# Performance work log

Measured on AMD Instinct MI355X. Metric: run time of the kernel, lower is better.

The kernel has to match this reference:

```python
import jax, jax.numpy as jnp
import numpy as np

N, T, DM = 8192, 32, 128   # nodes, patches, d_model (d_in = T*DM = 4096)
M, NNZ = 1024, 131072      # hyperedges, incidences
EPS = 1e-5
SLOPE = 0.2


def _bn(x, g, b, axes):
    # BatchNorm with batch statistics (training-mode math, eval dropout)
    m = jnp.mean(x, axis=axes, keepdims=True)
    v = jnp.var(x, axis=axes, keepdims=True)
    return (x - m) / jnp.sqrt(v + EPS) * g + b


def _hconv(x, he_attr, he_n, he_e, W, att, bias, heads):
    # PyG HypergraphConv, use_attention=True, attention_mode='node', concat=False
    out = W.shape[1] // heads
    xt = (x @ W).reshape(N, heads, out)          # [N, H, F]
    et = (he_attr @ W).reshape(M, heads, out)    # [M, H, F]
    xi = xt[he_n]                                # [nnz, H, F] gather node feats
    ej = et[he_e]                                # [nnz, H, F] gather edge feats
    alpha = jnp.sum(jnp.concatenate([xi, ej], axis=-1) * att, axis=-1)  # [nnz, H]
    alpha = jax.nn.leaky_relu(alpha, SLOPE)
    # segment softmax grouped by hyperedge (attention_mode='node')
    amax = jax.ops.segment_max(alpha, he_e, num_segments=M)
    ex = jnp.exp(alpha - amax[he_e])
    alpha = ex / jax.ops.segment_sum(ex, he_e, num_segments=M)[he_e]
    # degree normalizers (hyperedge_weight == 1)
    ones = jnp.ones((NNZ,), x.dtype)
    Dn = jax.ops.segment_sum(ones, he_n, num_segments=N)
    Dinv = jnp.where(Dn > 0, 1.0 / Dn, 0.0)
    Bm = jax.ops.segment_sum(ones, he_e, num_segments=M)
    Binv = jnp.where(Bm > 0, 1.0 / Bm, 0.0)
    # node -> edge, then edge -> node message passing
    eo = jax.ops.segment_sum(alpha[:, :, None] * Binv[he_e][:, None, None] * xi,
                             he_e, num_segments=M)                     # [M, H, F]
    no = jax.ops.segment_sum(alpha[:, :, None] * Dinv[he_n][:, None, None] * eo[he_e],
                             he_n, num_segments=N)                     # [N, H, F]
    return no.mean(axis=1) + bias  # concat=False -> mean over heads


def setup_inputs() -> dict:
    key = jax.random.key(0)
    ks = jax.random.split(key, 16)
    d_in = T * DM
    s = 0.02
    inp = {
        "x": jax.random.normal(ks[0], (N, T, DM), jnp.float32),
        "he_nodes": jax.random.randint(ks[1], (NNZ,), 0, N),
        "he_edges": jax.random.randint(ks[2], (NNZ,), 0, M),
        "W1": jax.random.normal(ks[3], (d_in, DM), jnp.float32) * s,
        "b1": jnp.zeros((DM,), jnp.float32),
        "g1": jnp.ones((DM,), jnp.float32), "be1": jnp.zeros((DM,), jnp.float32),
        "Wh1": jax.random.normal(ks[4], (DM, 4 * DM), jnp.float32) * s,
        "att1": jax.random.normal(ks[5], (1, 4, 2 * DM), jnp.float32) * s,
        "bh1": jnp.zeros((DM,), jnp.float32),
        "g2": jnp.ones((DM,), jnp.float32), "be2": jnp.zeros((DM,), jnp.float32),
        "Wh2": jax.random.normal(ks[6], (DM, DM), jnp.float32) * s,
        "att2": jax.random.normal(ks[7], (1, 1, 2 * DM), jnp.float32) * s,
        "bh2": jnp.zeros((DM,), jnp.float32),
        "g3": jnp.ones((DM,), jnp.float32), "be3": jnp.zeros((DM,), jnp.float32),
        "W3": jax.random.normal(ks[8], (DM, d_in), jnp.float32) * s,
        "b3": jnp.zeros((d_in,), jnp.float32),
        "g4": jnp.ones((DM,), jnp.float32), "be4": jnp.zeros((DM,), jnp.float32),
    }
    return inp


def reference(x, he_nodes, he_edges, W1, b1, g1, be1, Wh1, att1, bh1,
              g2, be2, Wh2, att2, bh2, g3, be3, W3, b3, g4, be4):
    src = x
    h = x.reshape(N, T * DM)
    h = jax.nn.leaky_relu(h @ W1 + b1, SLOPE)
    h = _bn(h, g1, be1, 0)
    # hyperedge_attr = incidence^T @ h  (== to_dense_adj(...).T @ h)
    he_attr = jax.ops.segment_sum(h[he_nodes], he_edges, num_segments=M)
    h = h + _hconv(h, he_attr, he_nodes, he_edges, Wh1, att1, bh1, 4)
    h = _bn(h, g2, be2, 0)
    he_attr = jax.ops.segment_sum(h[he_nodes], he_edges, num_segments=M)
    h = h + _hconv(h, he_attr, he_nodes, he_edges, Wh2, att2, bh2, 1)
    h = _bn(h, g3, be3, 0)
    h = jax.nn.leaky_relu(h @ W3 + b3, SLOPE)
    h = src + h.reshape(N, T, DM)
    h = _bn(h, g4, be4, (0, 1))  # BN over channel DM, stats over (N, T)
    return h
```

## Files before the change

kernel.cpp:

```cpp
#include <hip/hip_runtime.h>
#include <hip/hip_bf16.h>
#include <math.h>

#define NN   8192
#define TT   32
#define DIN  4096
#define MME  1024
#define NNZK 131072
#define EPSV 1e-5f
#define MALL (NN + MME)
#define NSLOT 8

typedef __attribute__((ext_vector_type(8))) short bf16x8;
typedef __attribute__((ext_vector_type(4))) float f32x4;

__device__ __forceinline__ float lrelu(float v){ return v > 0.f ? v : 0.2f*v; }
__device__ __forceinline__ short f2b(float f){
    union { __hip_bfloat16 h; short s; } u; u.h = __float2bfloat16(f); return u.s;
}
__device__ __forceinline__ float b2f(short s){
    union { float f; unsigned u; } u; u.u = ((unsigned)(unsigned short)s) << 16; return u.f;
}

__global__ void zero_i(int* p, int n){ int i = blockIdx.x*256 + threadIdx.x; if (i < n) p[i] = 0; }
__global__ void zero_f(float* p, int n){ int i = blockIdx.x*256 + threadIdx.x; if (i < n) p[i] = 0.f; }

__global__ void count_seg(const int* __restrict__ he_n, const int* __restrict__ he_e,
                          int* __restrict__ ncnt, int* __restrict__ ecnt){
    int k = blockIdx.x*256 + threadIdx.x;
    if (k < NNZK){ atomicAdd(&ecnt[he_e[k]], 1); atomicAdd(&ncnt[he_n[k]], 1); }
}

__global__ void scan_excl(const int* __restrict__ cnt, int* __restrict__ off,
                          int* __restrict__ cur, int n){
    int t = threadIdx.x;
    int lane = t & 63, wv = t >> 6;
    int chunk = n >> 10;
    int base = t*chunk;
    int s = 0;
#pragma unroll 4
    for (int i = 0; i < chunk; i++) s += cnt[base+i];
    int v = s;
    for (int d = 1; d < 64; d <<= 1){
        int u = __shfl_up(v, d);
        if (lane >= d) v += u;
    }
    __shared__ int wsum[16];
    if (lane == 63) wsum[wv] = v;
    __syncthreads();
    if (wv == 0 && lane < 16){
        int w2 = wsum[lane];
        for (int d = 1; d < 16; d <<= 1){
            int u = __shfl_up(w2, d);
            if (lane >= d) w2 += u;
        }
        wsum[lane] = w2;
    }
    __syncthreads();
    int excl = v - s + (wv > 0 ? wsum[wv-1] : 0);
    for (int i = 0; i < chunk; i++){
        off[base+i] = excl;
        cur[base+i] = excl;
        excl += cnt[base+i];
    }
    if (t == 1023) off[n] = excl;
}

__global__ void fill_perm2(const int* __restrict__ seg, const int* __restrict__ other,
                           int* __restrict__ cur, int* __restrict__ perm, int* __restrict__ oth){
    int k = blockIdx.x*256 + threadIdx.x;
    if (k < NNZK){
        int p = atomicAdd(&cur[seg[k]], 1);
        perm[p] = k;
        oth[p] = other[k];
    }
}

__global__ __launch_bounds__(256) void convert_x(const float4* __restrict__ x,
                                                 bf16x8* __restrict__ xb, int n8){
    int stride = gridDim.x*256;
    for (int i = blockIdx.x*256 + threadIdx.x; i < n8; i += stride){
        float4 lo = x[2*i], hi = x[2*i+1];
        bf16x8 v;
        v[0]=f2b(lo.x); v[1]=f2b(lo.y); v[2]=f2b(lo.z); v[3]=f2b(lo.w);
        v[4]=f2b(hi.x); v[5]=f2b(hi.y); v[6]=f2b(hi.z); v[7]=f2b(hi.w);
        xb[i] = v;
    }
}

__global__ void wconv_t(const float* __restrict__ W, __hip_bfloat16* __restrict__ BT, int K, int N){
    __shared__ float tile[32][33];
    int k0 = blockIdx.y*32, n0 = blockIdx.x*32;
    int tx = threadIdx.x & 31, ty = threadIdx.x >> 5;
    for (int i = ty; i < 32; i += 8) tile[i][tx] = W[(size_t)(k0+i)*N + n0+tx];
    __syncthreads();
    for (int i = ty; i < 32; i += 8)
        BT[(size_t)(n0+i)*K + k0 + tx] = __float2bfloat16(tile[tx][i]);
}

#define SWZ(b) ((b) ^ ((((b) >> 6) & 7) << 4))

__global__ __launch_bounds__(256) void gemm_bb(
    const __hip_bfloat16* __restrict__ Ab, const __hip_bfloat16* __restrict__ Bwt,
    __hip_bfloat16* __restrict__ Cb, int M, int N, int K, int kchunk)
{
    __shared__ f32x4 WsRaw[512];
    __shared__ f32x4 XsRaw[512];
    char* Ws = (char*)WsRaw;
    char* Xs = (char*)XsRaw;
    const int tid = threadIdx.x;
    const int lane = tid & 63;
    const int w = tid >> 6;
    const int m0 = blockIdx.y << 7, n0 = blockIdx.x << 7;
    const int kz = blockIdx.z * kchunk;
    const int wN = (w >> 1) << 6, wM = (w & 1) << 6;

    const int s0 = tid, s1 = tid + 256;
    const int r0 = s0 >> 2, k0b = (s0 & 3) << 3;
    const int r1 = s1 >> 2, k1b = (s1 & 3) << 3;
    const __hip_bfloat16* pA0 = Ab + (size_t)(m0 + r0)*K + kz + k0b;
    const __hip_bfloat16* pA1 = Ab + (size_t)(m0 + r1)*K + kz + k1b;
    const __hip_bfloat16* pW0 = Bwt + (size_t)(n0 + r0)*K + kz + k0b;
    const __hip_bfloat16* pW1 = Bwt + (size_t)(n0 + r1)*K + kz + k1b;
    const int wo0 = SWZ(s0 << 4), wo1 = SWZ(s1 << 4);

    int rwOff[4], rxOff[4];
#pragma unroll
    for (int f = 0; f < 4; f++){
        rwOff[f] = SWZ((wN + f*16 + (lane & 15))*64 + ((lane >> 4) << 4));
        rxOff[f] = SWZ((wM + f*16 + (lane & 15))*64 + ((lane >> 4) << 4));
// ... 16 lines not shown
            pA0 += 32; pA1 += 32; pW0 += 32; pW1 += 32;
            a0 = *(const bf16x8*)pA0; a1 = *(const bf16x8*)pA1;
            w0 = *(const bf16x8*)pW0; w1 = *(const bf16x8*)pW1;
        }
        bf16x8 wf[4], xf[4];
#pragma unroll
        for (int f = 0; f < 4; f++){
            wf[f] = *(const bf16x8*)(Ws + rwOff[f]);
            xf[f] = *(const bf16x8*)(Xs + rxOff[f]);
        }
#pragma unroll
        for (int i = 0; i < 4; i++)
#pragma unroll
            for (int j = 0; j < 4; j++)
                acc[i][j] = __builtin_amdgcn_mfma_f32_16x16x32_bf16(wf[i], xf[j], acc[i][j], 0, 0, 0);
    }

    const int mc = wM + (lane & 15);
    const int ncb = wN + ((lane >> 4) << 2);
    __hip_bfloat16* Cz = Cb + (size_t)blockIdx.z * ((size_t)M * (size_t)N);
#pragma unroll
    for (int j = 0; j < 4; j++){
        int row = m0 + mc + j*16;
#pragma unroll
        for (int i = 0; i < 4; i++){
            int col = n0 + ncb + i*16;
            f32x4 v = acc[i][j];
            short4 sv = { f2b(v[0]), f2b(v[1]), f2b(v[2]), f2b(v[3]) };
            *(short4*)&Cz[(size_t)row*N + col] = sv;
        }
    }
}

template<int MODE>
__global__ __launch_bounds__(256) void gemm_nt(
    const float* __restrict__ Aact, const __hip_bfloat16* __restrict__ Bwt,
    __hip_bfloat16* __restrict__ Cb, const float* __restrict__ bias,
    const float* __restrict__ coefA, int M, int N, int K, int kchunk)
{
    __shared__ f32x4 WsRaw[512];
    __shared__ f32x4 XsRaw[512];
    char* Ws = (char*)WsRaw;
    char* Xs = (char*)XsRaw;
    const int tid = threadIdx.x;
    const int lane = tid & 63;
    const int w = tid >> 6;
    const int m0 = blockIdx.y << 7, n0 = blockIdx.x << 7;
    const int wN = (w >> 1) << 6, wM = (w & 1) << 6;

    const int s0 = tid, s1 = tid + 256;
    const int r0 = s0 >> 2, k0b = (s0 & 3) << 3;
    const int r1 = s1 >> 2, k1b = (s1 & 3) << 3;
    const float* pX0 = Aact + (size_t)(m0 + r0)*K + k0b;
    const float* pX1 = Aact + (size_t)(m0 + r1)*K + k1b;
    const __hip_bfloat16* pW0 = Bwt + (size_t)(n0 + r0)*K + k0b;
    const __hip_bfloat16* pW1 = Bwt + (size_t)(n0 + r1)*K + k1b;
    const int wo0 = SWZ(s0 << 4), wo1 = SWZ(s1 << 4);

    int rwOff[4], rxOff[4];
#pragma unroll
    for (int f = 0; f < 4; f++){
        rwOff[f] = SWZ((wN + f*16 + (lane & 15))*64 + ((lane >> 4) << 4));
        rxOff[f] = SWZ((wM + f*16 + (lane & 15))*64 + ((lane >> 4) << 4));
    }

    f32x4 acc[4][4] = {};

    float4 x0l = *(const float4*)pX0, x0h = *(const float4*)(pX0+4);
    float4 x1l = *(const float4*)pX1, x1h = *(const float4*)(pX1+4);
    bf16x8 w0 = *(const bf16x8*)pW0, w1 = *(const bf16x8*)pW1;

    const int nsteps = kchunk >> 5;
    for (int ks = 0; ks < nsteps; ks++){
        if (MODE == 7){
            int kc0 = k0b + ks*32, kc1 = k1b + ks*32;
            float4 s0v = *(const float4*)&coefA[kc0],     s0w = *(const float4*)&coefA[kc0+4];
            float4 h0v = *(const float4*)&coefA[128+kc0], h0w = *(const float4*)&coefA[128+kc0+4];
            float4 s1v = *(const float4*)&coefA[kc1],     s1w = *(const float4*)&coefA[kc1+4];
            float4 h1v = *(const float4*)&coefA[128+kc1], h1w = *(const float4*)&coefA[128+kc1+4];
            x0l.x = x0l.x*s0v.x + h0v.x; x0l.y = x0l.y*s0v.y + h0v.y;
            x0l.z = x0l.z*s0v.z + h0v.z; x0l.w = x0l.w*s0v.w + h0v.w;
            x0h.x = x0h.x*s0w.x + h0w.x; x0h.y = x0h.y*s0w.y + h0w.y;
            x0h.z = x0h.z*s0w.z + h0w.z; x0h.w = x0h.w*s0w.w + h0w.w;
            x1l.x = x1l.x*s1v.x + h1v.x; x1l.y = x1l.y*s1v.y + h1v.y;
            x1l.z = x1l.z*s1v.z + h1v.z; x1l.w = x1l.w*s1v.w + h1v.w;
            x1h.x = x1h.x*s1w.x + h1w.x; x1h.y = x1h.y*s1w.y + h1w.y;
            x1h.z = x1h.z*s1w.z + h1w.z; x1h.w = x1h.w*s1w.w + h1w.w;
        }
        bf16x8 vx0, vx1;
        vx0[0]=f2b(x0l.x); vx0[1]=f2b(x0l.y); vx0[2]=f2b(x0l.z); vx0[3]=f2b(x0l.w);
        vx0[4]=f2b(x0h.x); vx0[5]=f2b(x0h.y); vx0[6]=f2b(x0h.z); vx0[7]=f2b(x0h.w);
        vx1[0]=f2b(x1l.x); vx1[1]=f2b(x1l.y); vx1[2]=f2b(x1l.z); vx1[3]=f2b(x1l.w);
        vx1[4]=f2b(x1h.x); vx1[5]=f2b(x1h.y); vx1[6]=f2b(x1h.z); vx1[7]=f2b(x1h.w);
        __syncthreads();
        *(bf16x8*)(Xs + wo0) = vx0;
        *(bf16x8*)(Xs + wo1) = vx1;
        *(bf16x8*)(Ws + wo0) = w0;
        *(bf16x8*)(Ws + wo1) = w1;
        __syncthreads();
        if (ks + 1 < nsteps){
            pX0 += 32; pX1 += 32; pW0 += 32; pW1 += 32;
            x0l = *(const float4*)pX0; x0h = *(const float4*)(pX0+4);
            x1l = *(const float4*)pX1; x1h = *(const float4*)(pX1+4);
            w0 = *(const bf16x8*)pW0;  w1 = *(const bf16x8*)pW1;
        }
        bf16x8 wf[4], xf[4];
#pragma unroll
        for (int f = 0; f < 4; f++){
            wf[f] = *(const bf16x8*)(Ws + rwOff[f]);
            xf[f] = *(const bf16x8*)(Xs + rxOff[f]);
        }
#pragma unroll
        for (int i = 0; i < 4; i++)
#pragma unroll
            for (int j = 0; j < 4; j++)
                acc[i][j] = __builtin_amdgcn_mfma_f32_16x16x32_bf16(wf[i], xf[j], acc[i][j], 0, 0, 0);
    }

    const int mc = wM + (lane & 15);
    const int ncb = wN + ((lane >> 4) << 2);
#pragma unroll
    for (int j = 0; j < 4; j++){
        int row = m0 + mc + j*16;
#pragma unroll
        for (int i = 0; i < 4; i++){
            int col = n0 + ncb + i*16;
            f32x4 v = acc[i][j];
            if (MODE == 7){
                float4 b4 = *(const float4*)&bias[col];
                short4 sv = { f2b(lrelu(v[0] + b4.x)), f2b(lrelu(v[1] + b4.y)),
                              f2b(lrelu(v[2] + b4.z)), f2b(lrelu(v[3] + b4.w)) };
                *(short4*)&Cb[(size_t)row*N + col] = sv;
            } else {
                short4 sv = { f2b(v[0]), f2b(v[1]), f2b(v[2]), f2b(v[3]) };
                *(short4*)&Cb[(size_t)row*N + col] = sv;
            }
        }
    }
}

__global__ void reduce8s(const __hip_bfloat16* __restrict__ part, const float* __restrict__ bias,
                         float* __restrict__ out, int nf4, int parts, float* __restrict__ slots){
    int tid = threadIdx.x;
    int i = blockIdx.x*256 + tid;
    const short4* p4 = (const short4*)part;
    short4 v0 = p4[i];
    float4 s = { b2f(v0.x), b2f(v0.y), b2f(v0.z), b2f(v0.w) };
    for (int z = 1; z < parts; z++){
        short4 p = p4[(size_t)z*nf4 + i];
        s.x += b2f(p.x); s.y += b2f(p.y); s.z += b2f(p.z); s.w += b2f(p.w);
    }
    int c0 = (i & 31) << 2;
    s.x = lrelu(s.x + bias[c0+0]); s.y = lrelu(s.y + bias[c0+1]);
    s.z = lrelu(s.z + bias[c0+2]); s.w = lrelu(s.w + bias[c0+3]);
    ((float4*)out)[i] = s;
    __shared__ float S[128], Q[128];
    if (tid < 128){ S[tid] = 0.f; Q[tid] = 0.f; }
    __syncthreads();
    atomicAdd(&S[c0+0], s.x); atomicAdd(&Q[c0+0], s.x*s.x);
    atomicAdd(&S[c0+1], s.y); atomicAdd(&Q[c0+1], s.y*s.y);
    atomicAdd(&S[c0+2], s.z); atomicAdd(&Q[c0+2], s.z*s.z);
    atomicAdd(&S[c0+3], s.w); atomicAdd(&Q[c0+3], s.w*s.w);
    __syncthreads();
    if (tid < 128){
        int slot = blockIdx.x & (NSLOT-1);
        atomicAdd(&slots[slot*256 + tid], S[tid]);
        atomicAdd(&slots[slot*256 + 128 + tid], Q[tid]);
    }
}
// ... 52 lines not shown
        hi.z = (b2f(xv[6]) + b2f(fv[6]))*sc[6] + sh[6];
        hi.w = (b2f(xv[7]) + b2f(fv[7]))*sc[7] + sh[7];
        out[2*i]   = lo;
        out[2*i+1] = hi;
    }
}

__global__ void bn_stats_v2(const float* __restrict__ x, float* __restrict__ slots, int rows){
    int cg = threadIdx.x & 31, rg = threadIdx.x >> 5;
    float4 s = {0,0,0,0}, q = {0,0,0,0};
    for (int r = blockIdx.x*8 + rg; r < rows; r += gridDim.x*8){
        float4 v = ((const float4*)x)[(size_t)r*32 + cg];
        s.x += v.x; q.x += v.x*v.x;
        s.y += v.y; q.y += v.y*v.y;
        s.z += v.z; q.z += v.z*v.z;
        s.w += v.w; q.w += v.w*v.w;
    }
    __shared__ float S[128], Q[128];
    if (threadIdx.x < 128){ S[threadIdx.x] = 0.f; Q[threadIdx.x] = 0.f; }
    __syncthreads();
    int c0 = cg << 2;
    atomicAdd(&S[c0+0], s.x); atomicAdd(&Q[c0+0], q.x);
    atomicAdd(&S[c0+1], s.y); atomicAdd(&Q[c0+1], q.y);
    atomicAdd(&S[c0+2], s.z); atomicAdd(&Q[c0+2], q.z);
    atomicAdd(&S[c0+3], s.w); atomicAdd(&Q[c0+3], q.w);
    __syncthreads();
    if (threadIdx.x < 128){
        int slot = blockIdx.x & (NSLOT-1);
        atomicAdd(&slots[slot*256 + threadIdx.x], S[threadIdx.x]);
        atomicAdd(&slots[slot*256 + 128 + threadIdx.x], Q[threadIdx.x]);
    }
}

__global__ void bn_finalize2(const float* __restrict__ slots, int nslots,
                             const float* __restrict__ g, const float* __restrict__ b,
                             float invR, float* __restrict__ coef){
    int c = threadIdx.x;
    float s = 0.f, q = 0.f;
    for (int k = 0; k < nslots; k++){ s += slots[k*256 + c]; q += slots[k*256 + 128 + c]; }
    float m = s*invR;
    float v = q*invR - m*m;
    float sc = g[c]*rsqrtf(v + EPSV);
    coef[c] = sc;
    coef[128 + c] = b[c] - m*sc;
}

__global__ void bn_apply4(float4* __restrict__ x, const float* __restrict__ coef, size_t n4){
    size_t i = (size_t)blockIdx.x*blockDim.x + threadIdx.x;
    size_t stride = (size_t)gridDim.x*blockDim.x;
    for (; i < n4; i += stride){
        int c0 = (int)(i & 31) * 4;
        float4 v = x[i];
        v.x = v.x*coef[c0+0] + coef[128+c0+0];
        v.y = v.y*coef[c0+1] + coef[128+c0+1];
        v.z = v.z*coef[c0+2] + coef[128+c0+2];
        v.w = v.w*coef[c0+3] + coef[128+c0+3];
        x[i] = v;
    }
}

__global__ void seg_sum_edge(const int* __restrict__ eoff, const int* __restrict__ enode,
                             const float* __restrict__ h, float* __restrict__ out){
    int m = blockIdx.x, c = threadIdx.x;
    int s0 = eoff[m], cnt = eoff[m+1] - s0;
    __shared__ int sn[128];
    float acc = 0.f;
    for (int base = 0; base < cnt; base += 128){
        int i = base + c;
        if (i < cnt) sn[c] = enode[s0+i];
        __syncthreads();
        int lim = min(128, cnt - base);
        for (int j = 0; j < lim; j++) acc += h[(size_t)sn[j]*128 + c];
        __syncthreads();
    }
    out[(size_t)m*128 + c] = acc;
}

__global__ void row_att4b(const __hip_bfloat16* __restrict__ xt, const float* __restrict__ att,
                          int aoff, float* __restrict__ out){
    int n = blockIdx.x, lane = threadIdx.x;
#pragma unroll
    for (int h = 0; h < 4; h++){
        const short* xr = (const short*)(xt + (size_t)n*512 + h*128);
        const float* ar = att + h*256 + aoff;
        unsigned u = *(const unsigned*)(xr + 2*lane);
        float s = b2f((short)(u & 0xffff))*ar[2*lane] + b2f((short)(u >> 16))*ar[2*lane+1];
        for (int d = 32; d > 0; d >>= 1) s += __shfl_down(s, d);
        if (lane == 0) out[n*4 + h] = s;
    }
}

__global__ void row_att1b(const __hip_bfloat16* __restrict__ xt, const float* __restrict__ att,
                          int aoff, float* __restrict__ out){
    int n = blockIdx.x, lane = threadIdx.x;
    const short* xr = (const short*)(xt + (size_t)n*128);
    const float* ar = att + aoff;
    unsigned u = *(const unsigned*)(xr + 2*lane);
    float s = b2f((short)(u & 0xffff))*ar[2*lane] + b2f((short)(u >> 16))*ar[2*lane+1];
    for (int d = 32; d > 0; d >>= 1) s += __shfl_down(s, d);
    if (lane == 0) out[n] = s;
}

template<int H>
__global__ void seg_softmax(const int* __restrict__ eoff, const int* __restrict__ eperm,
                            const int* __restrict__ enode,
                            const float* __restrict__ ax, const float* __restrict__ ae,
                            float* __restrict__ alpha){
    int m = blockIdx.x, t = threadIdx.x;
    int s0 = eoff[m], cnt = eoff[m+1] - s0;
    if (cnt == 0) return;
    __shared__ float red[128];
    float aeh[H];
#pragma unroll
    for (int h = 0; h < H; h++) aeh[h] = ae[m*H + h];
    float lmax[H];
#pragma unroll
    for (int h = 0; h < H; h++) lmax[h] = -1e30f;
    for (int i = t; i < cnt; i += 128){
        int k = eperm[s0+i]; int n = enode[s0+i];
#pragma unroll
        for (int h = 0; h < H; h++){
            float v = lrelu(ax[n*H + h] + aeh[h]);
            alpha[(size_t)k*H + h] = v;
            lmax[h] = fmaxf(lmax[h], v);
        }
    }
    float gmax[H];
#pragma unroll
    for (int h = 0; h < H; h++){
        red[t] = lmax[h]; __syncthreads();
        for (int s = 64; s > 0; s >>= 1){ if (t < s) red[t] = fmaxf(red[t], red[t+s]); __syncthreads(); }
        gmax[h] = red[0]; __syncthreads();
    }
    float lsum[H];
#pragma unroll
    for (int h = 0; h < H; h++) lsum[h] = 0.f;
    for (int i = t; i < cnt; i += 128){
        int k = eperm[s0+i];
#pragma unroll
        for (int h = 0; h < H; h++){
            float ex = __expf(alpha[(size_t)k*H + h] - gmax[h]);
            alpha[(size_t)k*H + h] = ex;
            lsum[h] += ex;
        }
    }
    float ginv[H];
#pragma unroll
    for (int h = 0; h < H; h++){
        red[t] = lsum[h]; __syncthreads();
        for (int s = 64; s > 0; s >>= 1){ if (t < s) red[t] += red[t+s]; __syncthreads(); }
        ginv[h] = 1.f/red[0]; __syncthreads();
    }
    for (int i = t; i < cnt; i += 128){
        int k = eperm[s0+i];
#pragma unroll
        for (int h = 0; h < H; h++) alpha[(size_t)k*H + h] *= ginv[h];
    }
}

__global__ void seg_eo4(const int* __restrict__ eoff, const int* __restrict__ eperm,
                        const int* __restrict__ enode,
                        const float* __restrict__ alpha, const __hip_bfloat16* __restrict__ xt,
                        float* __restrict__ eo){
    int m = blockIdx.x;
    int t = threadIdx.x;
    int h = t >> 6, c2 = t & 63;
    int s0 = eoff[m], cnt = eoff[m+1] - s0;
    __shared__ int sn[128];
    __shared__ float sa[128][4];
    float acc0 = 0.f, acc1 = 0.f;
    for (int base = 0; base < cnt; base += 128){
        int i = base + t;
        if (t < 128 && i < cnt){
            int k = eperm[s0+i];
            sn[t] = enode[s0+i];
#pragma unroll
            for (int hh = 0; hh < 4; hh++) sa[t][hh] = alpha[(size_t)k*4 + hh];
        }
        __syncthreads();
        int lim = min(128, cnt - base);
#pragma unroll 4
        for (int j = 0; j < lim; j++){
            unsigned u = *(const unsigned*)((const short*)xt + (size_t)sn[j]*512 + h*128 + 2*c2);
            float a = sa[j][h];
            acc0 += a * b2f((short)(u & 0xffff));
            acc1 += a * b2f((short)(u >> 16));
        }
        __syncthreads();
    }
    float binv = cnt > 0 ? 1.f/(float)cnt : 0.f;
    float2 st = { acc0*binv, acc1*binv };
    *(float2*)&eo[(size_t)m*512 + h*128 + 2*c2] = st;
}

__global__ void seg_eo1b(const int* __restrict__ eoff, const int* __restrict__ eperm,
                         const int* __restrict__ enode,
                         const float* __restrict__ alpha, const __hip_bfloat16* __restrict__ xt,
                         float* __restrict__ eo){
    int m = blockIdx.x, c = threadIdx.x;
    int s0 = eoff[m], cnt = eoff[m+1] - s0;
    __shared__ int sn[128];
    __shared__ float sa[128];
    float acc = 0.f;
    for (int base = 0; base < cnt; base += 128){
        int i = base + c;
        if (i < cnt){
            sn[c] = enode[s0+i];
            sa[c] = alpha[eperm[s0+i]];
        }
        __syncthreads();
        int lim = min(128, cnt - base);
#pragma unroll 4
        for (int j = 0; j < lim; j++)
            acc += sa[j]*b2f(((const short*)xt)[(size_t)sn[j]*128 + c]);
        __syncthreads();
    }
    float binv = cnt > 0 ? 1.f/(float)cnt : 0.f;
    eo[(size_t)m*128 + c] = acc*binv;
}

template<int H>
__global__ void seg_node_out(const int* __restrict__ noff, const int* __restrict__ nperm,
                             const int* __restrict__ nedge,
                             const float* __restrict__ alpha, const float* __restrict__ eo,
                             const float* __restrict__ hin, const float* __restrict__ bias,
                             float* __restrict__ hout){
    int n = blockIdx.x, c = threadIdx.x;
    int s0 = noff[n], cnt = noff[n+1] - s0;
    float acc = 0.f;
    for (int i = 0; i < cnt; i++){
        int k = nperm[s0+i]; int e = nedge[s0+i];
        const float* er = eo + (size_t)e*(128*H);
#pragma unroll
        for (int h = 0; h < H; h++) acc += alpha[(size_t)k*H + h]*er[h*128 + c];
    }
    float dinv = cnt > 0 ? 1.f/((float)cnt*(float)H) : 0.f;
    hout[(size_t)n*128 + c] = hin[(size_t)n*128 + c] + bias[c] + acc*dinv;
}

extern "C" void kernel_launch(void* const* d_in, const int* in_sizes, int n_in,
                              void* d_out, int out_size, void* d_ws, size_t ws_size,
                              hipStream_t stream){
    const float* x    = (const float*)d_in[0];
    const int*   he_n = (const int*)  d_in[1];
    const int*   he_e = (const int*)  d_in[2];
    const float* W1   = (const float*)d_in[3];
    const float* b1   = (const float*)d_in[4];
    const float* g1   = (const float*)d_in[5];
    const float* be1  = (const float*)d_in[6];
    const float* Wh1  = (const float*)d_in[7];
    const float* att1 = (const float*)d_in[8];
    const float* bh1  = (const float*)d_in[9];
    const float* g2   = (const float*)d_in[10];
    const float* be2  = (const float*)d_in[11];
    const float* Wh2  = (const float*)d_in[12];
    const float* att2 = (const float*)d_in[13];
    const float* bh2  = (const float*)d_in[14];
    const float* g3   = (const float*)d_in[15];
    const float* be3  = (const float*)d_in[16];
    const float* W3   = (const float*)d_in[17];
    const float* b3   = (const float*)d_in[18];
    const float* g4   = (const float*)d_in[19];
    const float* be4  = (const float*)d_in[20];
    float* out = (float*)d_out;

    char* ws = (char*)d_ws;
    size_t off = 0;
    auto alloc = [&](size_t bytes)->char*{ char* p = ws + off; off += (bytes + 255) & ~(size_t)255; return p; };

// ... 2 lines not shown
    __hip_bfloat16* part = (__hip_bfloat16*)big;
    __hip_bfloat16* xt1b = (__hip_bfloat16*)(big + (size_t)16*NN*128*2);
    __hip_bfloat16* xbuf = (__hip_bfloat16*)alloc((size_t)NN*DIN*2);

    float* hall1  = (float*)alloc((size_t)MALL*128*4);
    float* hall2  = (float*)alloc((size_t)MALL*128*4);
    float* h3     = (float*)alloc((size_t)NN*128*4);
    __hip_bfloat16* xt2b = (__hip_bfloat16*)alloc((size_t)MALL*128*2);
    float* eo     = (float*)alloc((size_t)MME*512*4);
    float* alpha  = (float*)alloc((size_t)NNZK*4*4);
    float* ax     = (float*)alloc((size_t)NN*4*4);
    float* ae     = (float*)alloc((size_t)MME*4*4);
    float* slots  = (float*)alloc((size_t)NSLOT*256*4);
    float* coef   = (float*)alloc(256*4);
    __hip_bfloat16* W1T  = (__hip_bfloat16*)alloc((size_t)128*DIN*2);
    __hip_bfloat16* Wh1T = (__hip_bfloat16*)alloc((size_t)512*128*2);
    __hip_bfloat16* Wh2T = (__hip_bfloat16*)alloc((size_t)128*128*2);
    __hip_bfloat16* W3T  = (__hip_bfloat16*)alloc((size_t)DIN*128*2);
    int* ecnt  = (int*)alloc(MME*4);
    int* ncnt  = (int*)alloc(NN*4);
    int* eoffb = (int*)alloc((MME+1)*4);
    int* ecur  = (int*)alloc(MME*4);
    int* noffb = (int*)alloc((NN+1)*4);
    int* ncur  = (int*)alloc(NN*4);
    int* eperm = (int*)alloc((size_t)NNZK*4);
    int* nperm = (int*)alloc((size_t)NNZK*4);
    int* enode = (int*)alloc((size_t)NNZK*4);
    int* nedge = (int*)alloc((size_t)NNZK*4);

    convert_x<<<2048, 256, 0, stream>>>((const float4*)x, (bf16x8*)xbuf, NN*DIN/8);

    zero_i<<<(MME+NN+255)/256, 256, 0, stream>>>(ecnt, MME+NN);
    count_seg<<<NNZK/256, 256, 0, stream>>>(he_n, he_e, ncnt, ecnt);
    scan_excl<<<1, 1024, 0, stream>>>(ecnt, eoffb, ecur, MME);
    scan_excl<<<1, 1024, 0, stream>>>(ncnt, noffb, ncur, NN);
    fill_perm2<<<NNZK/256, 256, 0, stream>>>(he_e, he_n, ecur, eperm, enode);
    fill_perm2<<<NNZK/256, 256, 0, stream>>>(he_n, he_e, ncur, nperm, nedge);

    wconv_t<<<dim3(128/32, DIN/32), 256, 0, stream>>>(W1,  W1T,  DIN, 128);
    wconv_t<<<dim3(512/32, 128/32), 256, 0, stream>>>(Wh1, Wh1T, 128, 512);
    wconv_t<<<dim3(128/32, 128/32), 256, 0, stream>>>(Wh2, Wh2T, 128, 128);
    wconv_t<<<dim3(DIN/32, 128/32), 256, 0, stream>>>(W3,  W3T,  128, DIN);

    gemm_bb<<<dim3(1, NN/128, 16), 256, 0, stream>>>(xbuf, W1T, part, NN, 128, DIN, DIN/16);
    zero_f<<<NSLOT, 256, 0, stream>>>(slots, NSLOT*256);
    reduce8s<<<NN*128/4/256, 256, 0, stream>>>(part, b1, hall1, NN*128/4, 16, slots);
    bn_finalize2<<<1, 128, 0, stream>>>(slots, NSLOT, g1, be1, 1.f/NN, coef);
    bn_apply4<<<1024, 256, 0, stream>>>((float4*)hall1, coef, (size_t)NN*32);

    seg_sum_edge<<<MME, 128, 0, stream>>>(eoffb, enode, hall1, hall1 + (size_t)NN*128);
    gemm_nt<5><<<dim3(512/128, MALL/128, 1), 256, 0, stream>>>(hall1, Wh1T, xt1b, nullptr, nullptr, MALL, 512, 128, 128);
    row_att4b<<<NN, 64, 0, stream>>>(xt1b, att1, 0, ax);
    row_att4b<<<MME, 64, 0, stream>>>(xt1b + (size_t)NN*512, att1, 128, ae);
    seg_softmax<4><<<MME, 128, 0, stream>>>(eoffb, eperm, enode, ax, ae, alpha);
    seg_eo4<<<MME, 256, 0, stream>>>(eoffb, eperm, enode, alpha, xt1b, eo);
    seg_node_out<4><<<NN, 128, 0, stream>>>(noffb, nperm, nedge, alpha, eo, hall1, bh1, hall2);
    zero_f<<<NSLOT, 256, 0, stream>>>(slots, NSLOT*256);
    bn_stats_v2<<<256, 256, 0, stream>>>(hall2, slots, NN);
    bn_finalize2<<<1, 128, 0, stream>>>(slots, NSLOT, g2, be2, 1.f/NN, coef);
    bn_apply4<<<1024, 256, 0, stream>>>((float4*)hall2, coef, (size_t)NN*32);

    seg_sum_edge<<<MME, 128, 0, stream>>>(eoffb, enode, hall2, hall2 + (size_t)NN*128);
    gemm_nt<5><<<dim3(1, MALL/128, 1), 256, 0, stream>>>(hall2, Wh2T, xt2b, nullptr, nullptr, MALL, 128, 128, 128);
    row_att1b<<<NN, 64, 0, stream>>>(xt2b, att2, 0, ax);
    row_att1b<<<MME, 64, 0, stream>>>(xt2b + (size_t)NN*128, att2, 128, ae);
    seg_softmax<1><<<MME, 128, 0, stream>>>(eoffb, eperm, enode, ax, ae, alpha);
    seg_eo1b<<<MME, 128, 0, stream>>>(eoffb, eperm, enode, alpha, xt2b, eo);
    seg_node_out<1><<<NN, 128, 0, stream>>>(noffb, nperm, nedge, alpha, eo, hall2, bh2, h3);

    zero_f<<<NSLOT, 256, 0, stream>>>(slots, NSLOT*256);
    bn_stats_v2<<<256, 256, 0, stream>>>(h3, slots, NN);
    bn_finalize2<<<1, 128, 0, stream>>>(slots, NSLOT, g3, be3, 1.f/NN, coef);

    gemm_nt<7><<<dim3(DIN/128, NN/128, 1), 256, 0, stream>>>(h3, W3T, fbuf, b3, coef, NN, DIN, 128, 128);
    zero_f<<<NSLOT, 256, 0, stream>>>(slots, NSLOT*256);
    final_stats<<<2048, 256, 0, stream>>>((const bf16x8*)xbuf, (const bf16x8*)fbuf, slots, NN*DIN/8);
    bn_finalize2<<<1, 128, 0, stream>>>(slots, NSLOT, g4, be4, 1.f/((float)NN*TT), coef);
    final_apply<<<2048, 256, 0, stream>>>((const bf16x8*)xbuf, (const bf16x8*)fbuf, coef, (float4*)out, NN*DIN/8);
}
```

Before: 521.2 us.

## Fuse attention scores into GEMM epilogue and merge setup kernel launches

Computes the per-row attention dot products inside the hyperedge GEMM epilogue, removing the separate row_att kernels. Merges the scan, permutation-fill and weight-transpose launches into single kernels, and zeroes the BN slots inside the finalize step instead of in separate launches. Segment-sum kernels are vectorized to float4 loads with partial-sum reduction through shared memory, and the multi-head edge output layout is transposed so the node-output kernel reads each edge's four heads as one float4. The epilogue adds shared-memory atomics, and the attention score is now taken from fp32 accumulators rather than the rounded bf16 values, so numerics shift slightly.

```diff
diff --git a/kernel.cpp b/kernel.cpp
--- a/kernel.cpp
+++ b/kernel.cpp
@@ -31,7 +31,7 @@
     if (k < NNZK){ atomicAdd(&ecnt[he_e[k]], 1); atomicAdd(&ncnt[he_n[k]], 1); }
 }
 
-__global__ void scan_excl(const int* __restrict__ cnt, int* __restrict__ off,
+__device__ void scan_body(const int* __restrict__ cnt, int* __restrict__ off,
                           int* __restrict__ cur, int n){
     int t = threadIdx.x;
     int lane = t & 63, wv = t >> 6;
@@ -66,13 +66,21 @@
     if (t == 1023) off[n] = excl;
 }
 
-__global__ void fill_perm2(const int* __restrict__ seg, const int* __restrict__ other,
-                           int* __restrict__ cur, int* __restrict__ perm, int* __restrict__ oth){
+__global__ void scan2(const int* ecnt, int* eoffb, int* ecur,
+                      const int* ncnt, int* noffb, int* ncur){
+    if (blockIdx.x == 0) scan_body(ecnt, eoffb, ecur, MME);
+    else                 scan_body(ncnt, noffb, ncur, NN);
+}
+
+__global__ void fill_both(const int* __restrict__ he_n, const int* __restrict__ he_e,
+                          int* __restrict__ ecur, int* __restrict__ ncur,
+                          int* __restrict__ eperm, int* __restrict__ enode,
+                          int* __restrict__ nperm, int* __restrict__ nedge){
     int k = blockIdx.x*256 + threadIdx.x;
     if (k < NNZK){
-        int p = atomicAdd(&cur[seg[k]], 1);
-        perm[p] = k;
-        oth[p] = other[k];
+        int e = he_e[k], n = he_n[k];
+        int p = atomicAdd(&ecur[e], 1); eperm[p] = k; enode[p] = n;
+        int q = atomicAdd(&ncur[n], 1); nperm[q] = k; nedge[q] = e;
     }
 }
 
@@ -88,14 +96,26 @@
     }
 }
 
-__global__ void wconv_t(const float* __restrict__ W, __hip_bfloat16* __restrict__ BT, int K, int N){
+__device__ void wconv_body(const float* __restrict__ W, __hip_bfloat16* __restrict__ BT,
+                           int K, int N, int gx, int gy){
     __shared__ float tile[32][33];
-    int k0 = blockIdx.y*32, n0 = blockIdx.x*32;
+    int k0 = gy*32, n0 = gx*32;
     int tx = threadIdx.x & 31, ty = threadIdx.x >> 5;
     for (int i = ty; i < 32; i += 8) tile[i][tx] = W[(size_t)(k0+i)*N + n0+tx];
     __syncthreads();
     for (int i = ty; i < 32; i += 8)
         BT[(size_t)(n0+i)*K + k0 + tx] = __float2bfloat16(tile[tx][i]);
+}
+
+__global__ void wconv_all(const float* W1, __hip_bfloat16* W1T,
+                          const float* Wh1, __hip_bfloat16* Wh1T,
+                          const float* Wh2, __hip_bfloat16* Wh2T,
+                          const float* W3, __hip_bfloat16* W3T){
+    int b = blockIdx.x;
+    if (b < 512)            wconv_body(W1,  W1T,  DIN, 128, b % 4,          b / 4);
+    else if (b < 576){ b -= 512; wconv_body(Wh1, Wh1T, 128, 512, b % 16, b / 16); }
+    else if (b < 592){ b -= 576; wconv_body(Wh2, Wh2T, 128, 128, b % 4,  b / 4); }
+    else             { b -= 592; wconv_body(W3,  W3T,  128, DIN, b % 128, b / 128); }
 }
 
 #define SWZ(b) ((b) ^ ((((b) >> 6) & 7) << 4))
@@ -178,11 +198,115 @@
     }
 }
 
-template<int MODE>
-__global__ __launch_bounds__(256) void gemm_nt(
+template<int H>
+__global__ __launch_bounds__(256) void gemm_att(
+    const float* __restrict__ Aact, const __hip_bfloat16* __restrict__ Bwt,
+    __hip_bfloat16* __restrict__ Cb, const float* __restrict__ attv,
+    float* __restrict__ axo, float* __restrict__ aeo, int M, int N, int K)
+{
+    __shared__ f32x4 WsRaw[512];
+    __shared__ f32x4 XsRaw[512];
+    __shared__ float sAx[128];
+    char* Ws = (char*)WsRaw;
+    char* Xs = (char*)XsRaw;
+    const int tid = threadIdx.x;
+    const int lane = tid & 63;
+    const int w = tid >> 6;
+    const int m0 = blockIdx.y << 7, n0 = blockIdx.x << 7;
+    const int wN = (w >> 1) << 6, wM = (w & 1) << 6;
+
+    const int s0 = tid, s1 = tid + 256;
+    const int r0 = s0 >> 2, k0b = (s0 & 3) << 3;
+    const int r1 = s1 >> 2, k1b = (s1 & 3) << 3;
+    const float* pX0 = Aact + (size_t)(m0 + r0)*K + k0b;
+    const float* pX1 = Aact + (size_t)(m0 + r1)*K + k1b;
+    const __hip_bfloat16* pW0 = Bwt + (size_t)(n0 + r0)*K + k0b;
+    const __hip_bfloat16* pW1 = Bwt + (size_t)(n0 + r1)*K + k1b;
+    const int wo0 = SWZ(s0 << 4), wo1 = SWZ(s1 << 4);
+
+    int rwOff[4], rxOff[4];
+#pragma unroll
+    for (int f = 0; f < 4; f++){
+        rwOff[f] = SWZ((wN + f*16 + (lane & 15))*64 + ((lane >> 4) << 4));
+        rxOff[f] = SWZ((wM + f*16 + (lane & 15))*64 + ((lane >> 4) << 4));
+    }
+
+    f32x4 acc[4][4] = {};
+
+    float4 x0l = *(const float4*)pX0, x0h = *(const float4*)(pX0+4);
+    float4 x1l = *(const float4*)pX1, x1h = *(const float4*)(pX1+4);
+    bf16x8 w0 = *(const bf16x8*)pW0, w1 = *(const bf16x8*)pW1;
+
+    const int nsteps = K >> 5;
+    for (int ks = 0; ks < nsteps; ks++){
+        bf16x8 vx0, vx1;
+        vx0[0]=f2b(x0l.x); vx0[1]=f2b(x0l.y); vx0[2]=f2b(x0l.z); vx0[3]=f2b(x0l.w);
+        vx0[4]=f2b(x0h.x); vx0[5]=f2b(x0h.y); vx0[6]=f2b(x0h.z); vx0[7]=f2b(x0h.w);
+        vx1[0]=f2b(x1l.x); vx1[1]=f2b(x1l.y); vx1[2]=f2b(x1l.z); vx1[3]=f2b(x1l.w);
+        vx1[4]=f2b(x1h.x); vx1[5]=f2b(x1h.y); vx1[6]=f2b(x1h.z); vx1[7]=f2b(x1h.w);
+        __syncthreads();
+        *(bf16x8*)(Xs + wo0) = vx0;
+        *(bf16x8*)(Xs + wo1) = vx1;
+        *(bf16x8*)(Ws + wo0) = w0;
+        *(bf16x8*)(Ws + wo1) = w1;
+        __syncthreads();
+        if (ks + 1 < nsteps){
+            pX0 += 32; pX1 += 32; pW0 += 32; pW1 += 32;
+            x0l = *(const float4*)pX0; x0h = *(const float4*)(pX0+4);
+            x1l = *(const float4*)pX1; x1h = *(const float4*)(pX1+4);
+            w0 = *(const bf16x8*)pW0;  w1 = *(const bf16x8*)pW1;
+        }
+        bf16x8 wf[4], xf[4];
+#pragma unroll
+        for (int f = 0; f < 4; f++){
+            wf[f] = *(const bf16x8*)(Ws + rwOff[f]);
+            xf[f] = *(const bf16x8*)(Xs + rxOff[f]);
+        }
+#pragma unroll
+        for (int i = 0; i < 4; i++)
+#pragma unroll
+            for (int j = 0; j < 4; j++)
+                acc[i][j] = __builtin_amdgcn_mfma_f32_16x16x32_bf16(wf[i], xf[j], acc[i][j], 0, 0, 0);
+    }
+
+    const int mc = wM + (lane & 15);
+    const int ncb = wN + ((lane >> 4) << 2);
+    if (tid < 128) sAx[tid] = 0.f;
+    __syncthreads();
+    const int h = blockIdx.x;
+    const int aoff = (m0 >= NN) ? 128 : 0;
+    const float* av = attv + h*256 + aoff;
+    float4 a4[4];
+#pragma unroll
+    for (int i = 0; i < 4; i++) a4[i] = *(const float4*)&av[ncb + i*16];
+    float sj[4] = {0.f, 0.f, 0.f, 0.f};
+#pragma unroll
+    for (int j = 0; j < 4; j++){
+        int row = m0 + mc + j*16;
+#pragma unroll
+        for (int i = 0; i < 4; i++){
+            int col = n0 + ncb + i*16;
+            f32x4 v = acc[i][j];
+            short4 sv = { f2b(v[0]), f2b(v[1]), f2b(v[2]), f2b(v[3]) };
+            *(short4*)&Cb[(size_t)row*N + col] = sv;
+            sj[j] += v[0]*a4[i].x + v[1]*a4[i].y + v[2]*a4[i].z + v[3]*a4[i].w;
+        }
+    }
+#pragma unroll
+    for (int j = 0; j < 4; j++) atomicAdd(&sAx[mc + j*16], sj[j]);
+    __syncthreads();
+    if (tid < 128){
+        int row = m0 + tid;
+        float val = sAx[tid];
+        if (row < NN) axo[row*H + h] = val;
+        else          aeo[(row - NN)*H + h] = val;
+    }
+}
+
+__global__ __launch_bounds__(256) void gemm_nt7(
     const float* __restrict__ Aact, const __hip_bfloat16* __restrict__ Bwt,
     __hip_bfloat16* __restrict__ Cb, const float* __restrict__ bias,
-    const float* __restrict__ coefA, int M, int N, int K, int kchunk)
+    const float* __restrict__ coefA, int M, int N, int K)
 {
     __shared__ f32x4 WsRaw[512];
     __shared__ f32x4 XsRaw[512];
@@ -216,23 +340,21 @@
     float4 x1l = *(const float4*)pX1, x1h = *(const float4*)(pX1+4);
     bf16x8 w0 = *(const bf16x8*)pW0, w1 = *(const bf16x8*)pW1;
 
-    const int nsteps = kchunk >> 5;
+    const int nsteps = K >> 5;
     for (int ks = 0; ks < nsteps; ks++){
-        if (MODE == 7){
-            int kc0 = k0b + ks*32, kc1 = k1b + ks*32;
-            float4 s0v = *(const float4*)&coefA[kc0],     s0w = *(const float4*)&coefA[kc0+4];
-            float4 h0v = *(const float4*)&coefA[128+kc0], h0w = *(const float4*)&coefA[128+kc0+4];
-            float4 s1v = *(const float4*)&coefA[kc1],     s1w = *(const float4*)&coefA[kc1+4];
-            float4 h1v = *(const float4*)&coefA[128+kc1], h1w = *(const float4*)&coefA[128+kc1+4];
-            x0l.x = x0l.x*s0v.x + h0v.x; x0l.y = x0l.y*s0v.y + h0v.y;
-            x0l.z = x0l.z*s0v.z + h0v.z; x0l.w = x0l.w*s0v.w + h0v.w;
-            x0h.x = x0h.x*s0w.x + h0w.x; x0h.y = x0h.y*s0w.y + h0w.y;
-            x0h.z = x0h.z*s0w.z + h0w.z; x0h.w = x0h.w*s0w.w + h0w.w;
-            x1l.x = x1l.x*s1v.x + h1v.x; x1l.y = x1l.y*s1v.y + h1v.y;
-            x1l.z = x1l.z*s1v.z + h1v.z; x1l.w = x1l.w*s1v.w + h1v.w;
-            x1h.x = x1h.x*s1w.x + h1w.x; x1h.y = x1h.y*s1w.y + h1w.y;
-            x1h.z = x1h.z*s1w.z + h1w.z; x1h.w = x1h.w*s1w.w + h1w.w;
-        }
+        int kc0 = k0b + ks*32, kc1 = k1b + ks*32;
+        float4 s0v = *(const float4*)&coefA[kc0],     s0w = *(const float4*)&coefA[kc0+4];
+        float4 h0v = *(const float4*)&coefA[128+kc0], h0w = *(const float4*)&coefA[128+kc0+4];
+        float4 s1v = *(const float4*)&coefA[kc1],     s1w = *(const float4*)&coefA[kc1+4];
+        float4 h1v = *(const float4*)&coefA[128+kc1], h1w = *(const float4*)&coefA[128+kc1+4];
+        x0l.x = x0l.x*s0v.x + h0v.x; x0l.y = x0l.y*s0v.y + h0v.y;
+        x0l.z = x0l.z*s0v.z + h0v.z; x0l.w = x0l.w*s0v.w + h0v.w;
+        x0h.x = x0h.x*s0w.x + h0w.x; x0h.y = x0h.y*s0w.y + h0w.y;
+        x0h.z = x0h.z*s0w.z + h0w.z; x0h.w = x0h.w*s0w.w + h0w.w;
+        x1l.x = x1l.x*s1v.x + h1v.x; x1l.y = x1l.y*s1v.y + h1v.y;
+        x1l.z = x1l.z*s1v.z + h1v.z; x1l.w = x1l.w*s1v.w + h1v.w;
+        x1h.x = x1h.x*s1w.x + h1w.x; x1h.y = x1h.y*s1w.y + h1w.y;
+        x1h.z = x1h.z*s1w.z + h1w.z; x1h.w = x1h.w*s1w.w + h1w.w;
         bf16x8 vx0, vx1;
         vx0[0]=f2b(x0l.x); vx0[1]=f2b(x0l.y); vx0[2]=f2b(x0l.z); vx0[3]=f2b(x0l.w);
         vx0[4]=f2b(x0h.x); vx0[5]=f2b(x0h.y); vx0[6]=f2b(x0h.z); vx0[7]=f2b(x0h.w);
@@ -272,15 +394,10 @@
         for (int i = 0; i < 4; i++){
             int col = n0 + ncb + i*16;
             f32x4 v = acc[i][j];
-            if (MODE == 7){
-                float4 b4 = *(const float4*)&bias[col];
-                short4 sv = { f2b(lrelu(v[0] + b4.x)), f2b(lrelu(v[1] + b4.y)),
-                              f2b(lrelu(v[2] + b4.z)), f2b(lrelu(v[3] + b4.w)) };
-                *(short4*)&Cb[(size_t)row*N + col] = sv;
-            } else {
-                short4 sv = { f2b(v[0]), f2b(v[1]), f2b(v[2]), f2b(v[3]) };
-                *(short4*)&Cb[(size_t)row*N + col] = sv;
-            }
+            float4 b4 = *(const float4*)&bias[col];
+            short4 sv = { f2b(lrelu(v[0] + b4.x)), f2b(lrelu(v[1] + b4.y)),
+                          f2b(lrelu(v[2] + b4.z)), f2b(lrelu(v[3] + b4.w)) };
+            *(short4*)&Cb[(size_t)row*N + col] = sv;
         }
     }
 }
@@ -399,12 +516,15 @@
     }
 }
 
-__global__ void bn_finalize2(const float* __restrict__ slots, int nslots,
-                             const float* __restrict__ g, const float* __restrict__ b,
-                             float invR, float* __restrict__ coef){
+__global__ void bn_finalize2z(float* __restrict__ slots, int nslots,
+                              const float* __restrict__ g, const float* __restrict__ b,
+                              float invR, float* __restrict__ coef){
     int c = threadIdx.x;
     float s = 0.f, q = 0.f;
-    for (int k = 0; k < nslots; k++){ s += slots[k*256 + c]; q += slots[k*256 + 128 + c]; }
+    for (int k = 0; k < nslots; k++){
+        s += slots[k*256 + c]; q += slots[k*256 + 128 + c];
+        slots[k*256 + c] = 0.f; slots[k*256 + 128 + c] = 0.f;
+    }
     float m = s*invR;
     float v = q*invR - m*m;
     float sc = g[c]*rsqrtf(v + EPSV);
@@ -428,44 +548,30 @@
 
 __global__ void seg_sum_edge(const int* __restrict__ eoff, const int* __restrict__ enode,
                              const float* __restrict__ h, float* __restrict__ out){
-    int m = blockIdx.x, c = threadIdx.x;
+    int m = blockIdx.x, t = threadIdx.x;
+    int jg = t >> 5, cq = t & 31;
     int s0 = eoff[m], cnt = eoff[m+1] - s0;
     __shared__ int sn[128];
-    float acc = 0.f;
+    __shared__ float4 comb[4][32];
+    float4 acc = {0,0,0,0};
     for (int base = 0; base < cnt; base += 128){
-        int i = base + c;
-        if (i < cnt) sn[c] = enode[s0+i];
+        int i = base + t;
+        if (i < cnt) sn[t] = enode[s0+i];
         __syncthreads();
         int lim = min(128, cnt - base);
-        for (int j = 0; j < lim; j++) acc += h[(size_t)sn[j]*128 + c];
-        __syncthreads();
-    }
-    out[(size_t)m*128 + c] = acc;
-}
-
-__global__ void row_att4b(const __hip_bfloat16* __restrict__ xt, const float* __restrict__ att,
-                          int aoff, float* __restrict__ out){
-    int n = blockIdx.x, lane = threadIdx.x;
-#pragma unroll
-    for (int h = 0; h < 4; h++){
-        const short* xr = (const short*)(xt + (size_t)n*512 + h*128);
-        const float* ar = att + h*256 + aoff;
-        unsigned u = *(const unsigned*)(xr + 2*lane);
-        float s = b2f((short)(u & 0xffff))*ar[2*lane] + b2f((short)(u >> 16))*ar[2*lane+1];
-        for (int d = 32; d > 0; d >>= 1) s += __shfl_down(s, d);
-        if (lane == 0) out[n*4 + h] = s;
-    }
-}
-
-__global__ void row_att1b(const __hip_bfloat16* __restrict__ xt, const float* __restrict__ att,
-                          int aoff, float* __restrict__ out){
-    int n = blockIdx.x, lane = threadIdx.x;
-    const short* xr = (const short*)(xt + (size_t)n*128);
-    const float* ar = att + aoff;
-    unsigned u = *(const unsigned*)(xr + 2*lane);
-    float s = b2f((short)(u & 0xffff))*ar[2*lane] + b2f((short)(u >> 16))*ar[2*lane+1];
-    for (int d = 32; d > 0; d >>= 1) s += __shfl_down(s, d);
-    if (lane == 0) out[n] = s;
+        for (int j = jg; j < lim; j += 4){
+            float4 v = *(const float4*)&h[(size_t)sn[j]*128 + cq*4];
+            acc.x += v.x; acc.y += v.y; acc.z += v.z; acc.w += v.w;
+        }
+        __syncthreads();
+    }
+    comb[jg][cq] = acc;
+    __syncthreads();
+    if (t < 32){
+        float4 a = comb[0][t], b = comb[1][t], c = comb[2][t], d = comb[3][t];
+        float4 tot = { a.x+b.x+c.x+d.x, a.y+b.y+c.y+d.y, a.z+b.z+c.z+d.z, a.w+b.w+c.w+d.w };
+        *(float4*)&out[(size_t)m*128 + t*4] = tot;
+    }
 }
 
 template<int H>
@@ -529,79 +635,114 @@
                         const int* __restrict__ enode,
                         const float* __restrict__ alpha, const __hip_bfloat16* __restrict__ xt,
                         float* __restrict__ eo){
-    int m = blockIdx.x;
-    int t = threadIdx.x;
-    int h = t >> 6, c2 = t & 63;
+    int m = blockIdx.x, t = threadIdx.x;
+    int jpar = t >> 7, cq = t & 127;
+    int hq = cq >> 5;
     int s0 = eoff[m], cnt = eoff[m+1] - s0;
     __shared__ int sn[128];
     __shared__ float sa[128][4];
-    float acc0 = 0.f, acc1 = 0.f;
+    __shared__ float comb[256][4];
+    float acc[4] = {0.f, 0.f, 0.f, 0.f};
     for (int base = 0; base < cnt; base += 128){
         int i = base + t;
         if (t < 128 && i < cnt){
-            int k = eperm[s0+i];
             sn[t] = enode[s0+i];
-#pragma unroll
-            for (int hh = 0; hh < 4; hh++) sa[t][hh] = alpha[(size_t)k*4 + hh];
+            *(float4*)sa[t] = *(const float4*)&alpha[(size_t)eperm[s0+i]*4];
         }
         __syncthreads();
         int lim = min(128, cnt - base);
-#pragma unroll 4
-        for (int j = 0; j < lim; j++){
-            unsigned u = *(const unsigned*)((const short*)xt + (size_t)sn[j]*512 + h*128 + 2*c2);
-            float a = sa[j][h];
-            acc0 += a * b2f((short)(u & 0xffff));
-            acc1 += a * b2f((short)(u >> 16));
-        }
-        __syncthreads();
-    }
-    float binv = cnt > 0 ? 1.f/(float)cnt : 0.f;
-    float2 st = { acc0*binv, acc1*binv };
-    *(float2*)&eo[(size_t)m*512 + h*128 + 2*c2] = st;
+        for (int j = jpar; j < lim; j += 2){
+            const ushort* p = (const ushort*)xt + (size_t)sn[j]*512 + cq*4;
+            ushort4 u = *(const ushort4*)p;
+            float a = sa[j][hq];
+            acc[0] += a*b2f((short)u.x); acc[1] += a*b2f((short)u.y);
+            acc[2] += a*b2f((short)u.z); acc[3] += a*b2f((short)u.w);
+        }
+        __syncthreads();
+    }
+    comb[t][0] = acc[0]; comb[t][1] = acc[1]; comb[t][2] = acc[2]; comb[t][3] = acc[3];
+    __syncthreads();
+    if (t < 128){
+        float binv = cnt > 0 ? 1.f/(float)cnt : 0.f;
+#pragma unroll
+        for (int i2 = 0; i2 < 4; i2++){
+            int ch = t*4 + i2;
+            int h = ch >> 7, c = ch & 127;
+            eo[(size_t)m*512 + c*4 + h] = (comb[t][i2] + comb[t+128][i2]) * binv;
+        }
+    }
 }
 
 __global__ void seg_eo1b(const int* __restrict__ eoff, const int* __restrict__ eperm,
                          const int* __restrict__ enode,
                          const float* __restrict__ alpha, const __hip_bfloat16* __restrict__ xt,
                          float* __restrict__ eo){
-    int m = blockIdx.x, c = threadIdx.x;
+    int m = blockIdx.x, t = threadIdx.x;
+    int jg = t >> 5, cq = t & 31;
     int s0 = eoff[m], cnt = eoff[m+1] - s0;
     __shared__ int sn[128];
     __shared__ float sa[128];
-    float acc = 0.f;
+    __shared__ float4 comb[4][32];
+    float4 acc = {0,0,0,0};
     for (int base = 0; base < cnt; base += 128){
-        int i = base + c;
+        int i = base + t;
         if (i < cnt){
-            sn[c] = enode[s0+i];
-            sa[c] = alpha[eperm[s0+i]];
+            sn[t] = enode[s0+i];
+            sa[t] = alpha[eperm[s0+i]];
         }
         __syncthreads();
         int lim = min(128, cnt - base);
-#pragma unroll 4
-        for (int j = 0; j < lim; j++)
-            acc += sa[j]*b2f(((const short*)xt)[(size_t)sn[j]*128 + c]);
-        __syncthreads();
-    }
-    float binv = cnt > 0 ? 1.f/(float)cnt : 0.f;
-    eo[(size_t)m*128 + c] = acc*binv;
-}
-
-template<int H>
-__global__ void seg_node_out(const int* __restrict__ noff, const int* __restrict__ nperm,
-                             const int* __restrict__ nedge,
-                             const float* __restrict__ alpha, const float* __restrict__ eo,
-                             const float* __restrict__ hin, const float* __restrict__ bias,
-                             float* __restrict__ hout){
+        for (int j = jg; j < lim; j += 4){
+            const ushort* p = (const ushort*)xt + (size_t)sn[j]*128 + cq*4;
+            ushort4 u = *(const ushort4*)p;
+            float a = sa[j];
+            acc.x += a*b2f((short)u.x); acc.y += a*b2f((short)u.y);
+            acc.z += a*b2f((short)u.z); acc.w += a*b2f((short)u.w);
+        }
+        __syncthreads();
+    }
+    comb[jg][cq] = acc;
+    __syncthreads();
+    if (t < 32){
+        float binv = cnt > 0 ? 1.f/(float)cnt : 0.f;
+        float4 a = comb[0][t], b = comb[1][t], c = comb[2][t], d = comb[3][t];
+        float4 tot = { (a.x+b.x+c.x+d.x)*binv, (a.y+b.y+c.y+d.y)*binv,
+                       (a.z+b.z+c.z+d.z)*binv, (a.w+b.w+c.w+d.w)*binv };
+        *(float4*)&eo[(size_t)m*128 + t*4] = tot;
+    }
+}
+
+__global__ void seg_node_out4(const int* __restrict__ noff, const int* __restrict__ nperm,
+                              const int* __restrict__ nedge,
+                              const float* __restrict__ alpha, const float* __restrict__ eo,
+                              const float* __restrict__ hin, const float* __restrict__ bias,
+                              float* __restrict__ hout){
     int n = blockIdx.x, c = threadIdx.x;
     int s0 = noff[n], cnt = noff[n+1] - s0;
     float acc = 0.f;
     for (int i = 0; i < cnt; i++){
         int k = nperm[s0+i]; int e = nedge[s0+i];
-        const float* er = eo + (size_t)e*(128*H);
-#pragma unroll
-        for (int h = 0; h < H; h++) acc += alpha[(size_t)k*H + h]*er[h*128 + c];
-    }
-    float dinv = cnt > 0 ? 1.f/((float)cnt*(float)H) : 0.f;
+        float4 al = *(const float4*)&alpha[(size_t)k*4];
+        float4 ev = *(const float4*)&eo[(size_t)e*512 + c*4];
+        acc += al.x*ev.x + al.y*ev.y + al.z*ev.z + al.w*ev.w;
+    }
+    float dinv = cnt > 0 ? 1.f/((float)cnt*4.f) : 0.f;
+    hout[(size_t)n*128 + c] = hin[(size_t)n*128 + c] + bias[c] + acc*dinv;
+}
+
+__global__ void seg_node_out1(const int* __restrict__ noff, const int* __restrict__ nperm,
+                              const int* __restrict__ nedge,
+                              const float* __restrict__ alpha, const float* __restrict__ eo,
+                              const float* __restrict__ hin, const float* __restrict__ bias,
+                              float* __restrict__ hout){
+    int n = blockIdx.x, c = threadIdx.x;
+    int s0 = noff[n], cnt = noff[n+1] - s0;
+    float acc = 0.f;
+    for (int i = 0; i < cnt; i++){
+        int k = nperm[s0+i]; int e = nedge[s0+i];
+        acc += alpha[k]*eo[(size_t)e*128 + c];
+    }
+    float dinv = cnt > 0 ? 1.f/(float)cnt : 0.f;
     hout[(size_t)n*128 + c] = hin[(size_t)n*128 + c] + bias[c] + acc*dinv;
 }
 
@@ -670,49 +811,37 @@
 
     zero_i<<<(MME+NN+255)/256, 256, 0, stream>>>(ecnt, MME+NN);
     count_seg<<<NNZK/256, 256, 0, stream>>>(he_n, he_e, ncnt, ecnt);
-    scan_excl<<<1, 1024, 0, stream>>>(ecnt, eoffb, ecur, MME);
-    scan_excl<<<1, 1024, 0, stream>>>(ncnt, noffb, ncur, NN);
-    fill_perm2<<<NNZK/256, 256, 0, stream>>>(he_e, he_n, ecur, eperm, enode);
-    fill_perm2<<<NNZK/256, 256, 0, stream>>>(he_n, he_e, ncur, nperm, nedge);
-
-    wconv_t<<<dim3(128/32, DIN/32), 256, 0, stream>>>(W1,  W1T,  DIN, 128);
-    wconv_t<<<dim3(512/32, 128/32), 256, 0, stream>>>(Wh1, Wh1T, 128, 512);
-    wconv_t<<<dim3(128/32, 128/32), 256, 0, stream>>>(Wh2, Wh2T, 128, 128);
-    wconv_t<<<dim3(DIN/32, 128/32), 256, 0, stream>>>(W3,  W3T,  128, DIN);
+    scan2<<<2, 1024, 0, stream>>>(ecnt, eoffb, ecur, ncnt, noffb, ncur);
+    fill_both<<<NNZK/256, 256, 0, stream>>>(he_n, he_e, ecur, ncur, eperm, enode, nperm, nedge);
+
+    wconv_all<<<1104, 256, 0, stream>>>(W1, W1T, Wh1, Wh1T, Wh2, Wh2T, W3, W3T);
 
     gemm_bb<<<dim3(1, NN/128, 16), 256, 0, stream>>>(xbuf, W1T, part, NN, 128, DIN, DIN/16);
     zero_f<<<NSLOT, 256, 0, stream>>>(slots, NSLOT*256);
     reduce8s<<<NN*128/4/256, 256, 0, stream>>>(part, b1, hall1, NN*128/4, 16, slots);
-    bn_finalize2<<<1, 128, 0, stream>>>(slots, NSLOT, g1, be1, 1.f/NN, coef);
+    bn_finalize2z<<<1, 128, 0, stream>>>(slots, NSLOT, g1, be1, 1.f/NN, coef);
     bn_apply4<<<1024, 256, 0, stream>>>((float4*)hall1, coef, (size_t)NN*32);
 
     seg_sum_edge<<<MME, 128, 0, stream>>>(eoffb, enode, hall1, hall1 + (size_t)NN*128);
-    gemm_nt<5><<<dim3(512/128, MALL/128, 1), 256, 0, stream>>>(hall1, Wh1T, xt1b, nullptr, nullptr, MALL, 512, 128, 128);
-    row_att4b<<<NN, 64, 0, stream>>>(xt1b, att1, 0, ax);
-    row_att4b<<<MME, 64, 0, stream>>>(xt1b + (size_t)NN*512, att1, 128, ae);
+    gemm_att<4><<<dim3(4, MALL/128), 256, 0, stream>>>(hall1, Wh1T, xt1b, att1, ax, ae, MALL, 512, 128);
     seg_softmax<4><<<MME, 128, 0, stream>>>(eoffb, eperm, enode, ax, ae, alpha);
     seg_eo4<<<MME, 256, 0, stream>>>(eoffb, eperm, enode, alpha, xt1b, eo);
-    seg_node_out<4><<<NN, 128, 0, stream>>>(noffb, nperm, nedge, alpha, eo, hall1, bh1, hall2);
-    zero_f<<<NSLOT, 256, 0, stream>>>(slots, NSLOT*256);
+    seg_node_out4<<<NN, 128, 0, stream>>>(noffb, nperm, nedge, alpha, eo, hall1, bh1, hall2);
     bn_stats_v2<<<256, 256, 0, stream>>>(hall2, slots, NN);
-    bn_finalize2<<<1, 128, 0, stream>>>(slots, NSLOT, g2, be2, 1.f/NN, coef);
+    bn_finalize2z<<<1, 128, 0, stream>>>(slots, NSLOT, g2, be2, 1.f/NN, coef);
     bn_apply4<<<1024, 256, 0, stream>>>((float4*)hall2, coef, (size_t)NN*32);
 
     seg_sum_edge<<<MME, 128, 0, stream>>>(eoffb, enode, hall2, hall2 + (size_t)NN*128);
-    gemm_nt<5><<<dim3(1, MALL/128, 1), 256, 0, stream>>>(hall2, Wh2T, xt2b, nullptr, nullptr, MALL, 128, 128, 128);
-    row_att1b<<<NN, 64, 0, stream>>>(xt2b, att2, 0, ax);
-    row_att1b<<<MME, 64, 0, stream>>>(xt2b + (size_t)NN*128, att2, 128, ae);
+    gemm_att<1><<<dim3(1, MALL/128), 256, 0, stream>>>(hall2, Wh2T, xt2b, att2, ax, ae, MALL, 128, 128);
     seg_softmax<1><<<MME, 128, 0, stream>>>(eoffb, eperm, enode, ax, ae, alpha);
     seg_eo1b<<<MME, 128, 0, stream>>>(eoffb, eperm, enode, alpha, xt2b, eo);
-    seg_node_out<1><<<NN, 128, 0, stream>>>(noffb, nperm, nedge, alpha, eo, hall2, bh2, h3);
-
-    zero_f<<<NSLOT, 256, 0, stream>>>(slots, NSLOT*256);
+    seg_node_out1<<<NN, 128, 0, stream>>>(noffb, nperm, nedge, alpha, eo, hall2, bh2, h3);
+
     bn_stats_v2<<<256, 256, 0, stream>>>(h3, slots, NN);
-    bn_finalize2<<<1, 128, 0, stream>>>(slots, NSLOT, g3, be3, 1.f/NN, coef);
-
-    gemm_nt<7><<<dim3(DIN/128, NN/128, 1), 256, 0, stream>>>(h3, W3T, fbuf, b3, coef, NN, DIN, 128, 128);
-    zero_f<<<NSLOT, 256, 0, stream>>>(slots, NSLOT*256);
+    bn_finalize2z<<<1, 128, 0, stream>>>(slots, NSLOT, g3, be3, 1.f/NN, coef);
+
+    gemm_nt7<<<dim3(DIN/128, NN/128), 256, 0, stream>>>(h3, W3T, fbuf, b3, coef, NN, DIN, 128);
     final_stats<<<2048, 256, 0, stream>>>((const bf16x8*)xbuf, (const bf16x8*)fbuf, slots, NN*DIN/8);
-    bn_finalize2<<<1, 128, 0, stream>>>(slots, NSLOT, g4, be4, 1.f/((float)NN*TT), coef);
+    bn_finalize2z<<<1, 128, 0, stream>>>(slots, NSLOT, g4, be4, 1.f/((float)NN*TT), coef);
     final_apply<<<2048, 256, 0, stream>>>((const bf16x8*)xbuf, (const bf16x8*)fbuf, coef, (float4*)out, NN*DIN/8);
 }
```

After: 490.0 us. -6.0%, faster.
